# Kernel optimization log

Hardware: AMD Instinct MI355X
Metric: run time of the kernel (lower is better)

Reference implementation:

```python
import jax, jax.numpy as jnp
import numpy as np

RHO = 1000.0  # seawater density used to convert wind stress to acceleration


def setup_inputs() -> dict:
    key = jax.random.key(0)
    k1, k2 = jax.random.split(key)
    Nforcing = 1440  # 60 days of hourly forcing
    TAx = (0.05 * jax.random.normal(k1, (Nforcing,), dtype=jnp.float32) + 0.08)
    TAy = 0.05 * jax.random.normal(k2, (Nforcing,), dtype=jnp.float32)
    pk = jnp.array([-3.9, -11.5], dtype=jnp.float32)  # K0 ~ 1/50m, K1 ~ 1e-5 s^-1
    fc = jnp.float32(1e-4)  # Coriolis frequency
    return {"pk": pk, "TAx": TAx, "TAy": TAy, "fc": fc,
            "t0": 0, "t1": 5184000, "dt": 60, "dt_forcing": 3600}


def _forward(pk, TAx, TAy, fc, t0, t1, dt, dt_forcing):
    nsub = dt_forcing // dt            # substeps per forcing step (static python int)
    Nf = (t1 - t0) // dt_forcing       # number of forcing steps
    n = TAx.shape[0]
    K = jnp.exp(pk)
    # Ekman (equilibrium) component, complex current Ce = K0*T / (K1 + i*fc)
    T = (TAx + 1j * TAy) / RHO
    Ce = K[0] * T / (K[1] + 1j * fc)
    Ue, Ve = jnp.real(Ce), jnp.imag(Ce)
    # NOTE: original uses self.dt (model dt, not dt_forcing) as gradient spacing
    dCedt = jnp.gradient(Ce, dt)
    dUedt, dVedt = jnp.real(dCedt), jnp.imag(dCedt)
    dtf = jnp.float32(dt)
    K1 = K[1]
    # interpolation weights aa = (it mod nsub)/nsub = iin/nsub, same for every outer step
    aas = jnp.arange(nsub, dtype=jnp.float32) / nsub

    def outer(carry, iout):
        # original: itsup = -1 if iout+1 >= len(TAx), which wraps to last element
        itsup = jnp.where(iout + 1 >= n, n - 1, iout + 1)
        dUe0, dUe1 = dUedt[iout], dUedt[itsup]
        dVe0, dVe1 = dVedt[iout], dVedt[itsup]

        def inner(c, aa):
            u, v = c
            dUe = (1.0 - aa) * dUe0 + aa * dUe1
            dVe = (1.0 - aa) * dVe0 + aa * dVe1
            du = -K1 * u + fc * v - dUe
            dv = -K1 * v - fc * u - dVe
            return (u + dtf * du, v + dtf * dv), None

        c, _ = jax.lax.scan(inner, carry, aas)
        return c, c

    init = (jnp.float32(0.0), jnp.float32(0.0))
    _, (us, vs) = jax.lax.scan(outer, init, jnp.arange(Nf))
    # original writes U[iout+1]: index Nf is out-of-bounds and dropped by .at[].set,
    # so the saved trajectory is the state shifted by one step with the last write dropped
    Unio = jnp.concatenate([jnp.zeros((1,), us.dtype), us[:-1]])
    Vnio = jnp.concatenate([jnp.zeros((1,), vs.dtype), vs[:-1]])
    return Ue + Unio, Ve + Vnio


def reference(pk, TAx, TAy, fc, t0, t1, dt, dt_forcing):
    return _forward(pk, TAx, TAy, fc, t0, t1, dt, dt_forcing)
```

## Files before the change

### kernel.cpp

```cpp
#include <hip/hip_runtime.h>


#define LSEG 24

__global__ __launch_bounds__(64, 1) void jslab_kernel(
        const float* __restrict__ pk,
        const float* __restrict__ TAx,
        const float* __restrict__ TAy,
        const float* __restrict__ fc_p,
        const int* __restrict__ dt_p,
        const int* __restrict__ dtf_p,
        float* __restrict__ out,
        int n, int Nf) {
    const int lane = threadIdx.x;

    const double K0  = exp((double)pk[0]);
    const double K1  = exp((double)pk[1]);
    const double fc  = (double)fc_p[0];
    const int    dt  = dt_p[0];
    const int    dtF = dtf_p[0];
    const int    nsub = dtF / dt;
    const double dtf = (double)dt;

    const double RHO = 1000.0;
    const double den = K1 * K1 + fc * fc;
    const double cfR =  K0 * K1 / (den * RHO);
    const double cfI = -K0 * fc / (den * RHO);

    const double Ar = 1.0 - dtf * K1;
    const double Ai = -dtf * fc;
    double Br = 1.0, Bi = 0.0;
    double s0r = 0.0, s0i = 0.0, s1r = 0.0, s1i = 0.0;
    for (int j = 0; j < nsub; ++j) {
        double aa = (double)((float)j / (float)nsub);
        double n0r = Ar * s0r - Ai * s0i + (1.0 - aa);
        double n0i = Ar * s0i + Ai * s0r;
        s0r = n0r; s0i = n0i;
        double n1r = Ar * s1r - Ai * s1i + aa;
        double n1i = Ar * s1i + Ai * s1r;
        s1r = n1r; s1i = n1i;
        double nbr = Br * Ar - Bi * Ai;
        double nbi = Br * Ai + Bi * Ar;
        Br = nbr; Bi = nbi;
    }
    const double P0r = -dtf * s0r, P0i = -dtf * s0i;
    const double P1r = -dtf * s1r, P1i = -dtf * s1i;

    const int base = lane * LSEG;

    auto ce = [&](int k, double& r, double& i) {
        k = k < 0 ? 0 : (k > n - 1 ? n - 1 : k);
        double tx = (double)TAx[k], ty = (double)TAy[k];
        r = tx * cfR - ty * cfI;
        i = tx * cfI + ty * cfR;
    };
    auto grad = [&](int k, double& gr, double& gi) {
        double ar, ai2, br2, bi2;
        if (k <= 0) {
            ce(1, ar, ai2); ce(0, br2, bi2);
            gr = (ar - br2) / dtf;        gi = (ai2 - bi2) / dtf;
        } else if (k >= n - 1) {
            ce(n - 1, ar, ai2); ce(n - 2, br2, bi2);
            gr = (ar - br2) / dtf;        gi = (ai2 - bi2) / dtf;
        } else {
            ce(k + 1, ar, ai2); ce(k - 1, br2, bi2);
            gr = (ar - br2) / (2.0 * dtf); gi = (ai2 - bi2) / (2.0 * dtf);
        }
    };

    double Fr[LSEG], Fi[LSEG];
    double pr = 0.0, pi = 0.0;
    #pragma unroll
    for (int j = 0; j < LSEG; ++j) {
        int i = base + j;
        double fr = 0.0, fi = 0.0;
        if (i < Nf) {
            int i0 = (i     < n) ? i     : n - 1;
            int i1 = (i + 1 < n) ? i + 1 : n - 1;
            double g0r, g0i, g1r, g1i;
            grad(i0, g0r, g0i);
            grad(i1, g1r, g1i);
            fr = P0r * g0r - P0i * g0i + P1r * g1r - P1i * g1i;
            fi = P0r * g0i + P0i * g0r + P1r * g1i + P1i * g1r;
        }
        Fr[j] = fr; Fi[j] = fi;
        double nr = Br * pr - Bi * pi + fr;
        double ni = Br * pi + Bi * pr + fi;
        pr = nr; pi = ni;
    }

    double wr, wi;
    {
        double t2r = Br * Br - Bi * Bi,     t2i = 2.0 * Br * Bi;
        double t3r = t2r * Br - t2i * Bi,   t3i = t2r * Bi + t2i * Br;
        double t6r = t3r * t3r - t3i * t3i, t6i = 2.0 * t3r * t3i;
        double tcr = t6r * t6r - t6i * t6i, tci = 2.0 * t6r * t6i;
        wr = tcr * tcr - tci * tci;         wi = 2.0 * tcr * tci;
    }

    double xr = pr, xi = pi;
    double cwr = wr, cwi = wi;
    #pragma unroll
    for (int d = 1; d < 64; d <<= 1) {
        double yr = __shfl_up(xr, d, 64);
        double yi = __shfl_up(xi, d, 64);
        if (lane >= d) {
            xr += cwr * yr - cwi * yi;
            xi += cwr * yi + cwi * yr;
        }
        double nr = cwr * cwr - cwi * cwi;
        double ni = 2.0 * cwr * cwi;
        cwr = nr; cwi = ni;
    }

    double sr = __shfl_up(xr, 1, 64);
    double si = __shfl_up(xi, 1, 64);
    if (lane == 0) { sr = 0.0; si = 0.0; }

    #pragma unroll
    for (int j = 0; j < LSEG; ++j) {
        int i = base + j;
        if (i < Nf) {
            double cer, cei;
            ce(i, cer, cei);
            out[i]      = (float)(cer + sr);
            out[Nf + i] = (float)(cei + si);
            double nr = Br * sr - Bi * si + Fr[j];
            double ni = Br * si + Bi * sr + Fi[j];
            sr = nr; si = ni;
        }
    }
}

extern "C" void kernel_launch(void* const* d_in, const int* in_sizes, int n_in,
                              void* d_out, int out_size, void* d_ws, size_t ws_size,
                              hipStream_t stream) {
    const float* pk   = (const float*)d_in[0];
    const float* TAx  = (const float*)d_in[1];
    const float* TAy  = (const float*)d_in[2];
    const float* fc   = (const float*)d_in[3];
    const int*   dt   = (const int*)d_in[6];
    const int*   dtF  = (const int*)d_in[7];
    float* out = (float*)d_out;

    const int n  = in_sizes[1];
    const int Nf = out_size / 2;

    jslab_kernel<<<dim3(1), dim3(64), 0, stream>>>(
        pk, TAx, TAy, fc, dt, dtF, out, n, Nf);
}
```

Before: 92.55 us.

## Compute forcing terms with 256 threads into shared memory before wave scan

```diff
diff --git a/kernel.cpp b/kernel.cpp
--- a/kernel.cpp
+++ b/kernel.cpp
@@ -2,8 +2,10 @@
 
 
 #define LSEG 24
+#define NSEG 64
+#define NT   256
 
-__global__ __launch_bounds__(64, 1) void jslab_kernel(
+__global__ __launch_bounds__(NT, 1) void jslab_kernel(
         const float* __restrict__ pk,
         const float* __restrict__ TAx,
         const float* __restrict__ TAy,
@@ -12,7 +14,10 @@
         const int* __restrict__ dtf_p,
         float* __restrict__ out,
         int n, int Nf) {
-    const int lane = threadIdx.x;
+    __shared__ double FR[NSEG * LSEG];
+    __shared__ double FI[NSEG * LSEG];
+
+    const int tid = threadIdx.x;
 
     const double K0  = exp((double)pk[0]);
     const double K1  = exp((double)pk[1]);
@@ -46,8 +51,6 @@
     const double P0r = -dtf * s0r, P0i = -dtf * s0i;
     const double P1r = -dtf * s1r, P1i = -dtf * s1i;
 
-    const int base = lane * LSEG;
-
     auto ce = [&](int k, double& r, double& i) {
         k = k < 0 ? 0 : (k > n - 1 ? n - 1 : k);
         double tx = (double)TAx[k], ty = (double)TAy[k];
@@ -68,66 +71,71 @@
         }
     };
 
-    double Fr[LSEG], Fi[LSEG];
-    double pr = 0.0, pi = 0.0;
-    #pragma unroll
-    for (int j = 0; j < LSEG; ++j) {
-        int i = base + j;
-        double fr = 0.0, fi = 0.0;
-        if (i < Nf) {
-            int i0 = (i     < n) ? i     : n - 1;
-            int i1 = (i + 1 < n) ? i + 1 : n - 1;
-            double g0r, g0i, g1r, g1i;
-            grad(i0, g0r, g0i);
-            grad(i1, g1r, g1i);
-            fr = P0r * g0r - P0i * g0i + P1r * g1r - P1i * g1i;
-            fi = P0r * g0i + P0i * g0r + P1r * g1i + P1i * g1r;
+    for (int i = tid; i < Nf; i += NT) {
+        int i0 = (i     < n) ? i     : n - 1;
+        int i1 = (i + 1 < n) ? i + 1 : n - 1;
+        double g0r, g0i, g1r, g1i;
+        grad(i0, g0r, g0i);
+        grad(i1, g1r, g1i);
+        FR[i] = P0r * g0r - P0i * g0i + P1r * g1r - P1i * g1i;
+        FI[i] = P0r * g0i + P0i * g0r + P1r * g1i + P1i * g1r;
+    }
+    for (int i = Nf + tid; i < NSEG * LSEG; i += NT) { FR[i] = 0.0; FI[i] = 0.0; }
+    __syncthreads();
+
+    if (tid < 64) {
+        const int lane = tid;
+        const int base = lane * LSEG;
+
+        double pr = 0.0, pi = 0.0;
+        #pragma unroll
+        for (int j = 0; j < LSEG; ++j) {
+            double fr = FR[base + j], fi = FI[base + j];
+            double nr = Br * pr - Bi * pi + fr;
+            double ni = Br * pi + Bi * pr + fi;
+            pr = nr; pi = ni;
         }
-        Fr[j] = fr; Fi[j] = fi;
-        double nr = Br * pr - Bi * pi + fr;
-        double ni = Br * pi + Bi * pr + fi;
-        pr = nr; pi = ni;
-    }
 
-    double wr, wi;
-    {
-        double t2r = Br * Br - Bi * Bi,     t2i = 2.0 * Br * Bi;
-        double t3r = t2r * Br - t2i * Bi,   t3i = t2r * Bi + t2i * Br;
-        double t6r = t3r * t3r - t3i * t3i, t6i = 2.0 * t3r * t3i;
-        double tcr = t6r * t6r - t6i * t6i, tci = 2.0 * t6r * t6i;
-        wr = tcr * tcr - tci * tci;         wi = 2.0 * tcr * tci;
-    }
+        double wr, wi;
+        {
+            double t2r = Br * Br - Bi * Bi,     t2i = 2.0 * Br * Bi;
+            double t3r = t2r * Br - t2i * Bi,   t3i = t2r * Bi + t2i * Br;
+            double t6r = t3r * t3r - t3i * t3i, t6i = 2.0 * t3r * t3i;
+            double tcr = t6r * t6r - t6i * t6i, tci = 2.0 * t6r * t6i;
+            wr = tcr * tcr - tci * tci;         wi = 2.0 * tcr * tci;
+        }
 
-    double xr = pr, xi = pi;
-    double cwr = wr, cwi = wi;
-    #pragma unroll
-    for (int d = 1; d < 64; d <<= 1) {
-        double yr = __shfl_up(xr, d, 64);
-        double yi = __shfl_up(xi, d, 64);
-        if (lane >= d) {
-            xr += cwr * yr - cwi * yi;
-            xi += cwr * yi + cwi * yr;
+        double xr = pr, xi = pi;
+        double cwr = wr, cwi = wi;
+        #pragma unroll
+        for (int d = 1; d < 64; d <<= 1) {
+            double yr = __shfl_up(xr, d, 64);
+            double yi = __shfl_up(xi, d, 64);
+            if (lane >= d) {
+                xr += cwr * yr - cwi * yi;
+                xi += cwr * yi + cwi * yr;
+            }
+            double nr = cwr * cwr - cwi * cwi;
+            double ni = 2.0 * cwr * cwi;
+            cwr = nr; cwi = ni;
         }
-        double nr = cwr * cwr - cwi * cwi;
-        double ni = 2.0 * cwr * cwi;
-        cwr = nr; cwi = ni;
-    }
 
-    double sr = __shfl_up(xr, 1, 64);
-    double si = __shfl_up(xi, 1, 64);
-    if (lane == 0) { sr = 0.0; si = 0.0; }
+        double sr = __shfl_up(xr, 1, 64);
+        double si = __shfl_up(xi, 1, 64);
+        if (lane == 0) { sr = 0.0; si = 0.0; }
 
-    #pragma unroll
-    for (int j = 0; j < LSEG; ++j) {
-        int i = base + j;
-        if (i < Nf) {
-            double cer, cei;
-            ce(i, cer, cei);
-            out[i]      = (float)(cer + sr);
-            out[Nf + i] = (float)(cei + si);
-            double nr = Br * sr - Bi * si + Fr[j];
-            double ni = Br * si + Bi * sr + Fi[j];
-            sr = nr; si = ni;
+        #pragma unroll
+        for (int j = 0; j < LSEG; ++j) {
+            int i = base + j;
+            if (i < Nf) {
+                double cer, cei;
+                ce(i, cer, cei);
+                out[i]      = (float)(cer + sr);
+                out[Nf + i] = (float)(cei + si);
+                double nr = Br * sr - Bi * si + FR[i];
+                double ni = Br * si + Bi * sr + FI[i];
+                sr = nr; si = ni;
+            }
         }
     }
 }
@@ -146,6 +154,6 @@
     const int n  = in_sizes[1];
     const int Nf = out_size / 2;
 
-    jslab_kernel<<<dim3(1), dim3(64), 0, stream>>>(
+    jslab_kernel<<<dim3(1), dim3(NT), 0, stream>>>(
         pk, TAx, TAy, fc, dt, dtF, out, n, Nf);
 }
```

Result: faster. 81.88 us (-11.5%).
